# Kernel optimization log

Hardware: AMD Instinct MI355X
Metric: run time of the kernel (lower is better)

The kernel has to match this reference:

```python
import jax, jax.numpy as jnp
import numpy as np

D_MODEL = 1024; D_STATE = 128; EXPAND = 2; HEADDIM = 64
D_INNER = EXPAND * D_MODEL; NHEADS = D_INNER // HEADDIM; PF = 2  # param_factor for complex
BATCH = 2; SEQ = 2048
DT_MIN = 0.001; DT_MAX = 0.1


def setup_inputs() -> dict:
    key = jax.random.key(0)
    k = jax.random.split(key, 10)
    u = jax.random.normal(k[0], (BATCH, SEQ, D_MODEL), jnp.float32)
    in_proj_w = jax.random.normal(k[1], (2 * D_INNER, D_MODEL), jnp.float32) * (D_MODEL ** -0.5)
    dt_projs_weight = jax.random.normal(k[2], (NHEADS, D_INNER), jnp.float32) * 0.02
    dt_projs_bias = (jax.random.uniform(k[3], (NHEADS,), jnp.float32)
                     * (np.log(DT_MAX) - np.log(DT_MIN)) + np.log(DT_MIN)).astype(jnp.float32)
    x_proj_w = jax.random.normal(k[4], (NHEADS * (1 + 2 * D_STATE * PF), D_INNER), jnp.float32) * (D_INNER ** -0.5)
    A = jnp.stack([-jax.random.uniform(k[5], (NHEADS, D_STATE), dtype=jnp.float32),
                   jax.random.normal(k[6], (NHEADS, D_STATE), jnp.float32) * 0.1], axis=-1)  # (H,N,2)
    D = jnp.ones((NHEADS,), jnp.float32)
    norm_B_w = jnp.ones((2 * D_STATE,), jnp.float32)
    norm_C_w = jnp.ones((2 * D_STATE,), jnp.float32)
    out_proj_w = jax.random.normal(k[7], (D_MODEL, D_INNER), jnp.float32) * (D_INNER ** -0.5)
    return {"u": u, "in_proj_w": in_proj_w, "dt_projs_weight": dt_projs_weight,
            "dt_projs_bias": dt_projs_bias, "x_proj_w": x_proj_w, "A": A, "D": D,
            "norm_B_w": norm_B_w, "norm_C_w": norm_C_w, "out_proj_w": out_proj_w}


def _rms_norm(x, w, eps=1e-6):
    return x * jax.lax.rsqrt(jnp.mean(x * x, axis=-1, keepdims=True) + eps) * w


def reference(u, in_proj_w, dt_projs_weight, dt_projs_bias, x_proj_w, A, D,
              norm_B_w, norm_C_w, out_proj_w):
    Bsz, L, _ = u.shape
    xz = u @ in_proj_w.T                        # (B,L,2*d_inner)
    x, z = jnp.split(xz, 2, axis=-1)
    x = jax.nn.silu(x)                          # (B,L,d_inner)
    dt = jax.nn.softplus(x @ dt_projs_weight.T + dt_projs_bias)  # (B,L,H)

    BCp = (x @ x_proj_w.T).reshape(Bsz, L, NHEADS, -1)
    BC = BCp[..., :2 * D_STATE * PF].reshape(Bsz, L, NHEADS, 2, D_STATE, PF)
    Bn = _rms_norm(BC[..., 0, :, :].reshape(Bsz, L, NHEADS, D_STATE * PF), norm_B_w)
    Cn = _rms_norm(BC[..., 1, :, :].reshape(Bsz, L, NHEADS, D_STATE * PF), norm_C_w)
    Bn = Bn.reshape(Bsz, L, NHEADS, D_STATE, PF)
    Cn = Cn.reshape(Bsz, L, NHEADS, D_STATE, PF)
    Bc = jax.lax.complex(Bn[..., 0], Bn[..., 1])  # (B,L,H,N) complex64
    Cc = jax.lax.complex(Cn[..., 0], Cn[..., 1])
    Ac = jax.lax.complex(A[..., 0], A[..., 1])    # (H,N) complex64

    xh = x.reshape(Bsz, L, NHEADS, HEADDIM)
    x_sum = xh.sum(axis=-1)                       # (B,L,H) -- kernel sums x_t over headdim
    zt = Ac[None, None] * (0.5 * dt)[..., None]   # (B,L,H,N) complex: A*dt/2
    den = 1.0 - zt
    abar = (1.0 + zt) / den                       # bilinear (Tustin) discretization
    u_in = Bc * ((dt * x_sum)[..., None] / den)   # Bbar * sum(x_t)

    def step(h, inp):
        a, b = inp
        h = a * h + b
        return h, h

    h0 = jnp.zeros((Bsz, NHEADS, D_STATE), jnp.complex64)
    _, hs = jax.lax.scan(step, h0, (jnp.swapaxes(abar, 0, 1), jnp.swapaxes(u_in, 0, 1)))
    hs = jnp.swapaxes(hs, 0, 1)                   # (B,L,H,N)
    y_red = jnp.real(Cc * hs).sum(axis=-1)        # (B,L,H), Re(C*h) reduced over state
    y = (xh * (y_red + D)[..., None]).reshape(Bsz, L, D_INNER)
    y = y * jax.nn.silu(z)
    return y @ out_proj_w.T
```

## Files before the change

### kernel.cpp

```cpp
#include <hip/hip_runtime.h>

#define BATCH   2
#define SEQ     2048
#define DMODEL  1024
#define DINNER  2048
#define NHEADS  32
#define HEADDIM 64
#define DSTATE  128
#define BLTOT   (BATCH * SEQ)
#define NCHUNK  32
#define CHUNK   64

#define OFF_UB   0ull
#define OFF_WXZ  8388608ull
#define OFF_WBC  16777216ull
#define OFF_WOUT 83886080ull
#define OFF_XB   88080384ull
#define OFF_YB   104857600ull
#define OFF_BC   121634816ull
#define OFF_SZ   255852544ull
#define OFF_DT   272629760ull
#define OFF_XS   273154048ull
#define OFF_CA   274202624ull
#define OFF_CS   276299776ull
#define OFF_HI   278396928ull
#define OFF_SS   280494080ull
#define OFF_P0   281542656ull
#define OFF_P1   298319872ull

typedef __attribute__((ext_vector_type(8))) short bf16x8;
typedef __attribute__((ext_vector_type(4))) float f32x4;

__device__ __forceinline__ float b2f(unsigned short u) {
    return __uint_as_float(((unsigned)u) << 16);
}
__device__ __forceinline__ unsigned short f2b(float f) {
    unsigned x = __float_as_uint(f);
    unsigned r = (x + 0x7fffu + ((x >> 16) & 1u)) >> 16;
    return (unsigned short)r;
}
__device__ __forceinline__ float silu_f(float v) {
    return v / (1.0f + __expf(-v));
}
__device__ __forceinline__ float softplus_f(float v) {
    return (v > 20.0f) ? v : log1pf(__expf(v));
}

__device__ __forceinline__ void gload_lds16(const void* g, void* l) {
    __builtin_amdgcn_global_load_lds(
        (const __attribute__((address_space(1))) unsigned int*)g,
        (__attribute__((address_space(3))) unsigned int*)l, 16, 0, 0);
}

__global__ __launch_bounds__(256) void conv_all_kernel(
    const float* __restrict__ u, const float* __restrict__ ipw,
    const float* __restrict__ opw, const float* __restrict__ xpw,
    unsigned short* __restrict__ u_b, unsigned short* __restrict__ w_xz,
    unsigned short* __restrict__ w_out, unsigned short* __restrict__ w_bc) {
    long idx = (long)blockIdx.x * 256 + threadIdx.x;
    if (idx >= 2621440L) {
        long e = (idx - 2621440L) * 4;
        long c = e >> 11, k = e & 2047;
        const float* s = xpw + ((c >> 9) * 513 + (c & 511)) * 2048 + k;
        float4 v = *(const float4*)s;
        ushort4 o = {f2b(v.x), f2b(v.y), f2b(v.z), f2b(v.w)};
        *(ushort4*)&w_bc[e] = o;
        return;
    }
    const float* src;
    unsigned short* dst;
    long i;
    if (idx < 1048576L)      { src = u;   dst = u_b;   i = idx; }
    else if (idx < 2097152L) { src = ipw; dst = w_xz;  i = idx - 1048576L; }
    else                     { src = opw; dst = w_out; i = idx - 2097152L; }
    float4 v = *(const float4*)&src[i * 4];
    ushort4 o = {f2b(v.x), f2b(v.y), f2b(v.z), f2b(v.w)};
    *(ushort4*)&dst[i * 4] = o;
}

template <int KTOT, int KLEN, int MODE>
__device__ __forceinline__ void gemm_body(
    const unsigned short* __restrict__ A, const unsigned short* __restrict__ B,
    void* __restrict__ C0, void* __restrict__ C1, float* __restrict__ C2,
    int N, int koff) {
    __shared__ short ldsA[128 * 64];
    __shared__ short ldsB[128 * 64];
    int tid = threadIdx.x;
    int row0 = blockIdx.y * 128, col0 = blockIdx.x * 128;
    int lane = tid & 63, wave = tid >> 6;
    int wrow = (wave >> 1) * 64, wcol = (wave & 1) * 64;
    int m = lane & 15, quad = lane >> 4;

    f32x4 acc[4][4];
#pragma unroll
    for (int i = 0; i < 4; ++i)
#pragma unroll
        for (int j = 0; j < 4; ++j) acc[i][j] = (f32x4){0.f, 0.f, 0.f, 0.f};

    int r = tid >> 2, c8 = (tid & 3) * 8;
    const unsigned short* Ag = A + (size_t)(row0 + r) * KTOT + koff + c8;
    const unsigned short* Bg = B + (size_t)(col0 + r) * KTOT + koff + c8;
    short* la = ldsA + tid * 8;
    short* lb = ldsB + tid * 8;

    for (int k0 = 0; k0 < KLEN; k0 += 64) {
#pragma unroll
        for (int p = 0; p < 4; ++p) {
            size_t goff = (size_t)(p >> 1) * 64 * KTOT + (p & 1) * 32 + k0;
            int loff = (p & 1) * 4096 + (p >> 1) * 2048;
            gload_lds16(Ag + goff, la + loff);
            gload_lds16(Bg + goff, lb + loff);
        }
        __syncthreads();
#pragma unroll
        for (int q = 0; q < 2; ++q) {
            bf16x8 af[4], bfr[4];
#pragma unroll
            for (int i = 0; i < 4; ++i)
                af[i] = *(const bf16x8*)
                    &ldsA[q * 4096 + (wrow + i * 16 + m) * 32 + quad * 8];
#pragma unroll
            for (int j = 0; j < 4; ++j)
                bfr[j] = *(const bf16x8*)
                    &ldsB[q * 4096 + (wcol + j * 16 + m) * 32 + quad * 8];
#pragma unroll
            for (int i = 0; i < 4; ++i)
#pragma unroll
                for (int j = 0; j < 4; ++j)
                    acc[i][j] = __builtin_amdgcn_mfma_f32_16x16x32_bf16(
                        af[i], bfr[j], acc[i][j], 0, 0, 0);
        }
        __syncthreads();
    }

    if (MODE == 1) {
        bool isx = (col0 < DINNER);
        if (isx) {
            int head = (col0 + wcol) >> 6;
            float ssum[4][4];
#pragma unroll
            for (int i = 0; i < 4; ++i)
#pragma unroll
                for (int reg = 0; reg < 4; ++reg) ssum[i][reg] = 0.f;
#pragma unroll
            for (int i = 0; i < 4; ++i)
#pragma unroll
                for (int reg = 0; reg < 4; ++reg) {
                    int row = row0 + wrow + i * 16 + quad * 4 + reg;
#pragma unroll
                    for (int j = 0; j < 4; ++j) {
                        int col = col0 + wcol + j * 16 + m;
                        float s = silu_f(acc[i][j][reg]);
                        ((unsigned short*)C0)[(size_t)row * DINNER + col] = f2b(s);
                        ssum[i][reg] += s;
                    }
                }
#pragma unroll
            for (int i = 0; i < 4; ++i)
#pragma unroll
                for (int reg = 0; reg < 4; ++reg) {
                    float s = ssum[i][reg];
                    s += __shfl_xor(s, 1);
                    s += __shfl_xor(s, 2);
                    s += __shfl_xor(s, 4);
                    s += __shfl_xor(s, 8);
                    if (m == 0) {
                        int row = row0 + wrow + i * 16 + quad * 4 + reg;
                        C2[(size_t)row * NHEADS + head] = s;
                    }
                }
        } else {
#pragma unroll
            for (int i = 0; i < 4; ++i)
#pragma unroll
                for (int reg = 0; reg < 4; ++reg) {
                    int row = row0 + wrow + i * 16 + quad * 4 + reg;
#pragma unroll
                    for (int j = 0; j < 4; ++j) {
                        int col = col0 + wcol + j * 16 + m - DINNER;
                        float s = silu_f(acc[i][j][reg]);
                        ((unsigned short*)C1)[(size_t)row * DINNER + col] = f2b(s);
                    }
                }
        }
    } else if (MODE == 2) {
        int hH = (col0 + wcol) >> 9;
        int w0 = (col0 + wcol) & 511;
#pragma unroll
        for (int i = 0; i < 4; ++i)
#pragma unroll
            for (int reg = 0; reg < 4; ++reg) {
                int row = row0 + wrow + i * 16 + quad * 4 + reg;
                unsigned short* dst =
                    (unsigned short*)C0 + ((size_t)hH * BLTOT + row) * 512 + w0;
#pragma unroll
                for (int j = 0; j < 4; ++j)
                    dst[j * 16 + m] = f2b(acc[i][j][reg]);
            }
    } else {
#pragma unroll
        for (int i = 0; i < 4; ++i)
#pragma unroll
            for (int reg = 0; reg < 4; ++reg) {
                int row = row0 + wrow + i * 16 + quad * 4 + reg;
#pragma unroll
                for (int j = 0; j < 4; ++j) {
                    int col = col0 + wcol + j * 16 + m;
                    ((float*)C0)[(size_t)row * N + col] = acc[i][j][reg];
                }
            }
    }
}

__global__ __launch_bounds__(256) void gemm_xz_kernel(
    const unsigned short* __restrict__ A, const unsigned short* __restrict__ B,
    void* C0, void* C1, float* C2) {
    gemm_body<1024, 1024, 1>(A, B, C0, C1, C2, 4096, 0);
}
__global__ __launch_bounds__(256) void gemm_bc_kernel(
    const unsigned short* __restrict__ A, const unsigned short* __restrict__ B,
    void* C0) {
    gemm_body<2048, 2048, 2>(A, B, C0, nullptr, nullptr, 16384, 0);
}
__global__ __launch_bounds__(256) void gemm_out_kernel(
    const unsigned short* __restrict__ A, const unsigned short* __restrict__ B,
    float* P0, float* P1) {
    float* dst = blockIdx.z ? P1 : P0;
    gemm_body<2048, 1024, 0>(A, B, dst, nullptr, nullptr, 1024,
                             blockIdx.z * 1024);
}

__global__ __launch_bounds__(256) void yout_reduce_kernel(
    const float* __restrict__ p0, const float* __restrict__ p1,
    float* __restrict__ out) {
    int i = (blockIdx.x * 256 + threadIdx.x) * 4;
    float4 a = *(const float4*)&p0[i];
    float4 b = *(const float4*)&p1[i];
    float4 o = {a.x + b.x, a.y + b.y, a.z + b.z, a.w + b.w};
    *(float4*)&out[i] = o;
}

__global__ __launch_bounds__(256) void dt_kernel(
    const unsigned short* __restrict__ x, const float* __restrict__ dtw,
    const float* __restrict__ dtb, float* __restrict__ dt) {
    __shared__ float xs[8][132];
    __shared__ float ws[32][132];
    int r0 = blockIdx.x * 8;
    int t = threadIdx.x;
    int lrow = t >> 5, lc4 = (t & 31) * 4;
    int lh = t >> 3, lc16 = (t & 7) * 16;
    int row = t >> 5, h = t & 31;
    float acc = 0.f;

    for (int kc = 0; kc < DINNER; kc += 128) {
        ushort4 a = *(const ushort4*)&x[(size_t)(r0 + lrow) * DINNER + kc + lc4];
        xs[lrow][lc4 + 0] = b2f(a.x); xs[lrow][lc4 + 1] = b2f(a.y);
        xs[lrow][lc4 + 2] = b2f(a.z); xs[lrow][lc4 + 3] = b2f(a.w);
#pragma unroll
        for (int q = 0; q < 4; ++q) {
            float4 w = *(const float4*)&dtw[(size_t)lh * DINNER + kc + lc16 + q * 4];
            *(float4*)&ws[lh][lc16 + q * 4] = w;
        }
        __syncthreads();
#pragma unroll
        for (int k = 0; k < 128; k += 4) {
            float4 xv = *(const float4*)&xs[row][k];
            float4 wv = *(const float4*)&ws[h][k];
            acc += xv.x * wv.x + xv.y * wv.y + xv.z * wv.z + xv.w * wv.w;
        }
        __syncthreads();
    }
    dt[(size_t)(r0 + row) * NHEADS + h] = softplus_f(acc + dtb[h]);
}

__global__ __launch_bounds__(256) void ss_kernel(
    const unsigned short* __restrict__ bct, float* __restrict__ ss) {
    int wgid = blockIdx.x * 4 + (threadIdx.x >> 6);
    int lane = threadIdx.x & 63;
    const unsigned short* p = bct + (size_t)wgid * 512 + lane * 8;
    ushort4 a = *(const ushort4*)p;
    ushort4 b = *(const ushort4*)(p + 4);
    float f0 = b2f(a.x), f1 = b2f(a.y), f2 = b2f(a.z), f3 = b2f(a.w);
    float f4 = b2f(b.x), f5 = b2f(b.y), f6 = b2f(b.z), f7 = b2f(b.w);
    float s = f0 * f0 + f1 * f1 + f2 * f2 + f3 * f3 +
              f4 * f4 + f5 * f5 + f6 * f6 + f7 * f7;
    s += __shfl_xor(s, 1);
    s += __shfl_xor(s, 2);
    s += __shfl_xor(s, 4);
    s += __shfl_xor(s, 8);
    s += __shfl_xor(s, 16);
    if ((lane & 31) == 0)
        ss[(size_t)wgid * 2 + (lane >> 5)] =
            rsqrtf(s * (1.0f / 256.0f) + 1e-6f);
}

__device__ __forceinline__ void coefs(
    float ar, float ai, float dtv, float xsv, float Br, float Bi,
    float& abr, float& abi, float& ur, float& ui) {
    float hd = 0.5f * dtv;
    float ztr = ar * hd, zti = ai * hd;
    float denr = 1.0f - ztr;
    float s2 = 1.0f / (denr * denr + zti * zti);
    float invr = denr * s2, invi = zti * s2;
    float opr = 1.0f + ztr;
    abr = opr * invr - zti * invi;
    abi = opr * invi + zti * invr;
    float coef = dtv * xsv;
    float cr = coef * invr, ci = coef * invi;
    ur = Br * cr - Bi * ci;
    ui = Br * ci + Bi * cr;
}

__global__ __launch_bounds__(64) void scan_pass1(
    const unsigned short* __restrict__ bct, const float* __restrict__ dt,
    const float* __restrict__ xsum, const float* __restrict__ A,
    const float* __restrict__ wB, const float* __restrict__ ss,
    float2* __restrict__ cA, float2* __restrict__ cS) {
    int blk = blockIdx.x;
    int bh = blk >> 5, c = blk & (NCHUNK - 1);
    int b = bh >> 5, h = bh & 31;
    int t = threadIdx.x;
    float4 av = *(const float4*)&A[(h * DSTATE + 2 * t) * 2];
    float4 wv = *(const float4*)&wB[4 * t];
    int l0 = c * CHUNK;
    size_t rbase = (size_t)h * BLTOT + b * SEQ + l0;
    const unsigned short* base = bct + rbase * 512;
    const float* ssp = ss + rbase * 2;
    const float* dtp = dt + (b * SEQ + l0) * NHEADS + h;
    const float* xsp = xsum + (b * SEQ + l0) * NHEADS + h;

    float pr0 = 1.f, pi0 = 0.f, sr0 = 0.f, si0 = 0.f;
    float pr1 = 1.f, pi1 = 0.f, sr1 = 0.f, si1 = 0.f;
    for (int l = 0; l < CHUNK; ++l) {
        uint2 bw = *(const uint2*)&base[(size_t)l * 512 + 4 * t];
        float scale = ssp[l * 2];
        float Br0 = b2f((unsigned short)(bw.x & 0xffff)) * scale * wv.x;
        float Bi0 = b2f((unsigned short)(bw.x >> 16)) * scale * wv.y;
        float Br1 = b2f((unsigned short)(bw.y & 0xffff)) * scale * wv.z;
        float Bi1 = b2f((unsigned short)(bw.y >> 16)) * scale * wv.w;
        float dtv = dtp[l * NHEADS], xsv = xsp[l * NHEADS];
        float abr, abi, ur, ui;
        coefs(av.x, av.y, dtv, xsv, Br0, Bi0, abr, abi, ur, ui);
        float ns = abr * sr0 - abi * si0 + ur;
        float nsi = abr * si0 + abi * sr0 + ui;
        sr0 = ns; si0 = nsi;
        float np = abr * pr0 - abi * pi0;
        float npi = abr * pi0 + abi * pr0;
        pr0 = np; pi0 = npi;
        coefs(av.z, av.w, dtv, xsv, Br1, Bi1, abr, abi, ur, ui);
        ns = abr * sr1 - abi * si1 + ur;
        nsi = abr * si1 + abi * sr1 + ui;
        sr1 = ns; si1 = nsi;
        np = abr * pr1 - abi * pi1;
        npi = abr * pi1 + abi * pr1;
        pr1 = np; pi1 = npi;
    }
    size_t idx = ((size_t)bh * NCHUNK + c) * DSTATE + 2 * t;
    *(float4*)&cA[idx] = (float4){pr0, pi0, pr1, pi1};
    *(float4*)&cS[idx] = (float4){sr0, si0, sr1, si1};
}

__global__ __launch_bounds__(128) void scan_fixup(
    const float2* __restrict__ cA, const float2* __restrict__ cS,
    float2* __restrict__ hin) {
    int bh = blockIdx.x;
    int n = threadIdx.x;
    float hr = 0.f, hi = 0.f;
    for (int c = 0; c < NCHUNK; ++c) {
        size_t idx = ((size_t)bh * NCHUNK + c) * DSTATE + n;
        hin[idx] = {hr, hi};
        float2 a = cA[idx];
        float2 s = cS[idx];
        float nhr = a.x * hr - a.y * hi + s.x;
        float nhi = a.x * hi + a.y * hr + s.y;
        hr = nhr; hi = nhi;
    }
}

__global__ __launch_bounds__(64) void scan_pass2(
    const unsigned short* __restrict__ bct, const float* __restrict__ dt,
    const float* __restrict__ xsum, const float* __restrict__ A,
    const float* __restrict__ wB, const float* __restrict__ wC,
    const float* __restrict__ ss, const float2* __restrict__ hin,
    const unsigned short* __restrict__ xb, const unsigned short* __restrict__ szb,
    const float* __restrict__ Dv, unsigned short* __restrict__ yb) {
    int blk = blockIdx.x;
    int bh = blk >> 5, c = blk & (NCHUNK - 1);
    int b = bh >> 5, h = bh & 31;
    int t = threadIdx.x;
    float4 av = *(const float4*)&A[(h * DSTATE + 2 * t) * 2];
    float4 wbv = *(const float4*)&wB[4 * t];
    float4 wcv = *(const float4*)&wC[4 * t];
    float Dh = Dv[h];
    int l0 = c * CHUNK;
    size_t rbase = (size_t)h * BLTOT + b * SEQ + l0;
    const unsigned short* base = bct + rbase * 512;
    const float* ssp = ss + rbase * 2;
    const float* dtp = dt + (b * SEQ + l0) * NHEADS + h;
    const float* xsp = xsum + (b * SEQ + l0) * NHEADS + h;
    size_t xoff0 = (size_t)(b * SEQ + l0) * DINNER + h * HEADDIM + t;

    float4 h0v = *(const float4*)&hin[((size_t)bh * NCHUNK + c) * DSTATE + 2 * t];
    float hr0 = h0v.x, hi0 = h0v.y, hr1 = h0v.z, hi1 = h0v.w;

    for (int l = 0; l < CHUNK; ++l) {
        uint2 bw = *(const uint2*)&base[(size_t)l * 512 + 4 * t];
        uint2 cw = *(const uint2*)&base[(size_t)l * 512 + 256 + 4 * t];
        float sB = ssp[l * 2 + 0];
        float sC = ssp[l * 2 + 1];
        float Br0 = b2f((unsigned short)(bw.x & 0xffff)) * sB * wbv.x;
        float Bi0 = b2f((unsigned short)(bw.x >> 16)) * sB * wbv.y;
        float Br1 = b2f((unsigned short)(bw.y & 0xffff)) * sB * wbv.z;
        float Bi1 = b2f((unsigned short)(bw.y >> 16)) * sB * wbv.w;
        float Cr0 = b2f((unsigned short)(cw.x & 0xffff)) * sC * wcv.x;
        float Ci0 = b2f((unsigned short)(cw.x >> 16)) * sC * wcv.y;
        float Cr1 = b2f((unsigned short)(cw.y & 0xffff)) * sC * wcv.z;
        float Ci1 = b2f((unsigned short)(cw.y >> 16)) * sC * wcv.w;
        float dtv = dtp[l * NHEADS], xsv = xsp[l * NHEADS];
        float abr, abi, ur, ui;
        coefs(av.x, av.y, dtv, xsv, Br0, Bi0, abr, abi, ur, ui);
        float nhr = abr * hr0 - abi * hi0 + ur;
        float nhi = abr * hi0 + abi * hr0 + ui;
        hr0 = nhr; hi0 = nhi;
        coefs(av.z, av.w, dtv, xsv, Br1, Bi1, abr, abi, ur, ui);
        nhr = abr * hr1 - abi * hi1 + ur;
        nhi = abr * hi1 + abi * hr1 + ui;
        hr1 = nhr; hi1 = nhi;
        float y = Cr0 * hr0 - Ci0 * hi0 + Cr1 * hr1 - Ci1 * hi1;
#pragma unroll
        for (int off = 1; off < 64; off <<= 1) y += __shfl_xor(y, off);
        size_t xo = xoff0 + (size_t)l * DINNER;
        float yr = y + Dh;
        float xv = b2f(xb[xo]);
        float zv = b2f(szb[xo]);
        yb[xo] = f2b(xv * yr * zv);
    }
}

extern "C" void kernel_launch(void* const* d_in, const int* in_sizes, int n_in,
                              void* d_out, int out_size, void* d_ws, size_t ws_size,
                              hipStream_t stream) {
    const float* u   = (const float*)d_in[0];
    const float* ipw = (const float*)d_in[1];
    const float* dtw = (const float*)d_in[2];
    const float* dtb = (const float*)d_in[3];
    const float* xpw = (const float*)d_in[4];
    const float* A   = (const float*)d_in[5];
    const float* Dv  = (const float*)d_in[6];
    const float* wB  = (const float*)d_in[7];
    const float* wC  = (const float*)d_in[8];
    const float* opw = (const float*)d_in[9];
    float* out = (float*)d_out;
    char* ws = (char*)d_ws;

    unsigned short* u_b   = (unsigned short*)(ws + OFF_UB);
    unsigned short* w_xz  = (unsigned short*)(ws + OFF_WXZ);
    unsigned short* w_bc  = (unsigned short*)(ws + OFF_WBC);
    unsigned short* w_out = (unsigned short*)(ws + OFF_WOUT);
    unsigned short* x_b   = (unsigned short*)(ws + OFF_XB);
    unsigned short* y_b   = (unsigned short*)(ws + OFF_YB);
    unsigned short* bct   = (unsigned short*)(ws + OFF_BC);
    unsigned short* sz    = (unsigned short*)(ws + OFF_SZ);
    float* dt    = (float*)(ws + OFF_DT);
    float* xsum  = (float*)(ws + OFF_XS);
    float2* cA   = (float2*)(ws + OFF_CA);
    float2* cS   = (float2*)(ws + OFF_CS);
    float2* hin  = (float2*)(ws + OFF_HI);
    float* ssbuf = (float*)(ws + OFF_SS);
    float* p0    = (float*)(ws + OFF_P0);
    float* p1    = (float*)(ws + OFF_P1);

    conv_all_kernel<<<43008, 256, 0, stream>>>(u, ipw, opw, xpw,
                                               u_b, w_xz, w_out, w_bc);

    gemm_xz_kernel<<<dim3(32, 32), 256, 0, stream>>>(u_b, w_xz, x_b, sz, xsum);
    dt_kernel<<<BLTOT / 8, 256, 0, stream>>>(x_b, dtw, dtb, dt);
    gemm_bc_kernel<<<dim3(128, 32), 256, 0, stream>>>(x_b, w_bc, bct);
    ss_kernel<<<NHEADS * BLTOT / 4, 256, 0, stream>>>(bct, ssbuf);

    scan_pass1<<<BATCH * NHEADS * NCHUNK, 64, 0, stream>>>(
        bct, dt, xsum, A, wB, ssbuf, cA, cS);
    scan_fixup<<<BATCH * NHEADS, 128, 0, stream>>>(cA, cS, hin);
    scan_pass2<<<BATCH * NHEADS * NCHUNK, 64, 0, stream>>>(
        bct, dt, xsum, A, wB, wC, ssbuf, hin, x_b, sz, Dv, y_b);

    gemm_out_kernel<<<dim3(8, 32, 2), 256, 0, stream>>>(y_b, w_out, p0, p1);
    yout_reduce_kernel<<<BLTOT * DMODEL / 4 / 256, 256, 0, stream>>>(p0, p1, out);
}
```

Measured before the change: 789.2 us.

## Split BC projection output into separate B and C planes and swap grid order

The B/C projection GEMM now writes B and C values into two separate planes (256 wide each) instead of one interleaved 512-wide row. Scan pass 1 reads only the B plane, so it no longer pulls C data into cache lines it never uses. The BC GEMM grid is also transposed so that consecutive blocks walk along rows of x for the same weight columns, which changes which operand tiles are reused in L2. The ss and scan kernels are updated to index the two planes.

```diff
diff --git a/kernel.cpp b/kernel.cpp
--- a/kernel.cpp
+++ b/kernel.cpp
@@ -17,7 +17,8 @@
 #define OFF_WOUT 83886080ull
 #define OFF_XB   88080384ull
 #define OFF_YB   104857600ull
-#define OFF_BC   121634816ull
+#define OFF_BCB  121634816ull
+#define OFF_BCC  188743680ull
 #define OFF_SZ   255852544ull
 #define OFF_DT   272629760ull
 #define OFF_XS   273154048ull
@@ -78,7 +79,7 @@
     *(ushort4*)&dst[i * 4] = o;
 }
 
-template <int KTOT, int KLEN, int MODE>
+template <int KTOT, int KLEN, int MODE, int SWAP>
 __device__ __forceinline__ void gemm_body(
     const unsigned short* __restrict__ A, const unsigned short* __restrict__ B,
     void* __restrict__ C0, void* __restrict__ C1, float* __restrict__ C2,
@@ -86,7 +87,8 @@
     __shared__ short ldsA[128 * 64];
     __shared__ short ldsB[128 * 64];
     int tid = threadIdx.x;
-    int row0 = blockIdx.y * 128, col0 = blockIdx.x * 128;
+    int row0 = (SWAP ? blockIdx.x : blockIdx.y) * 128;
+    int col0 = (SWAP ? blockIdx.y : blockIdx.x) * 128;
     int lane = tid & 63, wave = tid >> 6;
     int wrow = (wave >> 1) * 64, wcol = (wave & 1) * 64;
     int m = lane & 15, quad = lane >> 4;
@@ -184,15 +186,19 @@
                 }
         }
     } else if (MODE == 2) {
-        int hH = (col0 + wcol) >> 9;
-        int w0 = (col0 + wcol) & 511;
+        int cc = col0 + wcol;
+        int hH = cc >> 9;
+        int w0 = cc & 511;
+        unsigned short* plane =
+            (w0 < 256) ? (unsigned short*)C0 : (unsigned short*)C1;
+        int wo = w0 & 255;
 #pragma unroll
         for (int i = 0; i < 4; ++i)
 #pragma unroll
             for (int reg = 0; reg < 4; ++reg) {
                 int row = row0 + wrow + i * 16 + quad * 4 + reg;
                 unsigned short* dst =
-                    (unsigned short*)C0 + ((size_t)hH * BLTOT + row) * 512 + w0;
+                    plane + ((size_t)hH * BLTOT + row) * 256 + wo;
 #pragma unroll
                 for (int j = 0; j < 4; ++j)
                     dst[j * 16 + m] = f2b(acc[i][j][reg]);
@@ -215,19 +221,19 @@
 __global__ __launch_bounds__(256) void gemm_xz_kernel(
     const unsigned short* __restrict__ A, const unsigned short* __restrict__ B,
     void* C0, void* C1, float* C2) {
-    gemm_body<1024, 1024, 1>(A, B, C0, C1, C2, 4096, 0);
+    gemm_body<1024, 1024, 1, 0>(A, B, C0, C1, C2, 4096, 0);
 }
 __global__ __launch_bounds__(256) void gemm_bc_kernel(
     const unsigned short* __restrict__ A, const unsigned short* __restrict__ B,
-    void* C0) {
-    gemm_body<2048, 2048, 2>(A, B, C0, nullptr, nullptr, 16384, 0);
+    void* Bp, void* Cp) {
+    gemm_body<2048, 2048, 2, 1>(A, B, Bp, Cp, nullptr, 16384, 0);
 }
 __global__ __launch_bounds__(256) void gemm_out_kernel(
     const unsigned short* __restrict__ A, const unsigned short* __restrict__ B,
     float* P0, float* P1) {
     float* dst = blockIdx.z ? P1 : P0;
-    gemm_body<2048, 1024, 0>(A, B, dst, nullptr, nullptr, 1024,
-                             blockIdx.z * 1024);
+    gemm_body<2048, 1024, 0, 0>(A, B, dst, nullptr, nullptr, 1024,
+                                blockIdx.z * 1024);
 }
 
 __global__ __launch_bounds__(256) void yout_reduce_kernel(
@@ -274,10 +280,12 @@
 }
 
 __global__ __launch_bounds__(256) void ss_kernel(
-    const unsigned short* __restrict__ bct, float* __restrict__ ss) {
+    const unsigned short* __restrict__ bcB, const unsigned short* __restrict__ bcC,
+    float* __restrict__ ss) {
     int wgid = blockIdx.x * 4 + (threadIdx.x >> 6);
     int lane = threadIdx.x & 63;
-    const unsigned short* p = bct + (size_t)wgid * 512 + lane * 8;
+    const unsigned short* plane = (lane < 32) ? bcB : bcC;
+    const unsigned short* p = plane + (size_t)wgid * 256 + (lane & 31) * 8;
     ushort4 a = *(const ushort4*)p;
     ushort4 b = *(const ushort4*)(p + 4);
     float f0 = b2f(a.x), f1 = b2f(a.y), f2 = b2f(a.z), f3 = b2f(a.w);
@@ -312,7 +320,7 @@
 }
 
 __global__ __launch_bounds__(64) void scan_pass1(
-    const unsigned short* __restrict__ bct, const float* __restrict__ dt,
+    const unsigned short* __restrict__ bcB, const float* __restrict__ dt,
     const float* __restrict__ xsum, const float* __restrict__ A,
     const float* __restrict__ wB, const float* __restrict__ ss,
     float2* __restrict__ cA, float2* __restrict__ cS) {
@@ -324,7 +332,7 @@
     float4 wv = *(const float4*)&wB[4 * t];
     int l0 = c * CHUNK;
     size_t rbase = (size_t)h * BLTOT + b * SEQ + l0;
-    const unsigned short* base = bct + rbase * 512;
+    const unsigned short* base = bcB + rbase * 256;
     const float* ssp = ss + rbase * 2;
     const float* dtp = dt + (b * SEQ + l0) * NHEADS + h;
     const float* xsp = xsum + (b * SEQ + l0) * NHEADS + h;
@@ -332,7 +340,7 @@
     float pr0 = 1.f, pi0 = 0.f, sr0 = 0.f, si0 = 0.f;
     float pr1 = 1.f, pi1 = 0.f, sr1 = 0.f, si1 = 0.f;
     for (int l = 0; l < CHUNK; ++l) {
-        uint2 bw = *(const uint2*)&base[(size_t)l * 512 + 4 * t];
+        uint2 bw = *(const uint2*)&base[(size_t)l * 256 + 4 * t];
         float scale = ssp[l * 2];
         float Br0 = b2f((unsigned short)(bw.x & 0xffff)) * scale * wv.x;
         float Bi0 = b2f((unsigned short)(bw.x >> 16)) * scale * wv.y;
@@ -378,12 +386,13 @@
 }
 
 __global__ __launch_bounds__(64) void scan_pass2(
-    const unsigned short* __restrict__ bct, const float* __restrict__ dt,
-    const float* __restrict__ xsum, const float* __restrict__ A,
-    const float* __restrict__ wB, const float* __restrict__ wC,
-    const float* __restrict__ ss, const float2* __restrict__ hin,
-    const unsigned short* __restrict__ xb, const unsigned short* __restrict__ szb,
-    const float* __restrict__ Dv, unsigned short* __restrict__ yb) {
+    const unsigned short* __restrict__ bcB, const unsigned short* __restrict__ bcC,
+    const float* __restrict__ dt, const float* __restrict__ xsum,
+    const float* __restrict__ A, const float* __restrict__ wB,
+    const float* __restrict__ wC, const float* __restrict__ ss,
+    const float2* __restrict__ hin, const unsigned short* __restrict__ xb,
+    const unsigned short* __restrict__ szb, const float* __restrict__ Dv,
+    unsigned short* __restrict__ yb) {
     int blk = blockIdx.x;
     int bh = blk >> 5, c = blk & (NCHUNK - 1);
     int b = bh >> 5, h = bh & 31;
@@ -394,7 +403,8 @@
     float Dh = Dv[h];
     int l0 = c * CHUNK;
     size_t rbase = (size_t)h * BLTOT + b * SEQ + l0;
-    const unsigned short* base = bct + rbase * 512;
+    const unsigned short* baseB = bcB + rbase * 256;
+    const unsigned short* baseC = bcC + rbase * 256;
     const float* ssp = ss + rbase * 2;
     const float* dtp = dt + (b * SEQ + l0) * NHEADS + h;
     const float* xsp = xsum + (b * SEQ + l0) * NHEADS + h;
@@ -404,8 +414,8 @@
     float hr0 = h0v.x, hi0 = h0v.y, hr1 = h0v.z, hi1 = h0v.w;
 
     for (int l = 0; l < CHUNK; ++l) {
-        uint2 bw = *(const uint2*)&base[(size_t)l * 512 + 4 * t];
-        uint2 cw = *(const uint2*)&base[(size_t)l * 512 + 256 + 4 * t];
+        uint2 bw = *(const uint2*)&baseB[(size_t)l * 256 + 4 * t];
+        uint2 cw = *(const uint2*)&baseC[(size_t)l * 256 + 4 * t];
         float sB = ssp[l * 2 + 0];
         float sC = ssp[l * 2 + 1];
         float Br0 = b2f((unsigned short)(bw.x & 0xffff)) * sB * wbv.x;
@@ -459,7 +469,8 @@
     unsigned short* w_out = (unsigned short*)(ws + OFF_WOUT);
     unsigned short* x_b   = (unsigned short*)(ws + OFF_XB);
     unsigned short* y_b   = (unsigned short*)(ws + OFF_YB);
-    unsigned short* bct   = (unsigned short*)(ws + OFF_BC);
+    unsigned short* bcB   = (unsigned short*)(ws + OFF_BCB);
+    unsigned short* bcC   = (unsigned short*)(ws + OFF_BCC);
     unsigned short* sz    = (unsigned short*)(ws + OFF_SZ);
     float* dt    = (float*)(ws + OFF_DT);
     float* xsum  = (float*)(ws + OFF_XS);
@@ -475,14 +486,14 @@
 
     gemm_xz_kernel<<<dim3(32, 32), 256, 0, stream>>>(u_b, w_xz, x_b, sz, xsum);
     dt_kernel<<<BLTOT / 8, 256, 0, stream>>>(x_b, dtw, dtb, dt);
-    gemm_bc_kernel<<<dim3(128, 32), 256, 0, stream>>>(x_b, w_bc, bct);
-    ss_kernel<<<NHEADS * BLTOT / 4, 256, 0, stream>>>(bct, ssbuf);
+    gemm_bc_kernel<<<dim3(32, 128), 256, 0, stream>>>(x_b, w_bc, bcB, bcC);
+    ss_kernel<<<NHEADS * BLTOT / 4, 256, 0, stream>>>(bcB, bcC, ssbuf);
 
     scan_pass1<<<BATCH * NHEADS * NCHUNK, 64, 0, stream>>>(
-        bct, dt, xsum, A, wB, ssbuf, cA, cS);
+        bcB, dt, xsum, A, wB, ssbuf, cA, cS);
     scan_fixup<<<BATCH * NHEADS, 128, 0, stream>>>(cA, cS, hin);
     scan_pass2<<<BATCH * NHEADS * NCHUNK, 64, 0, stream>>>(
-        bct, dt, xsum, A, wB, wC, ssbuf, hin, x_b, sz, Dv, y_b);
+        bcB, bcC, dt, xsum, A, wB, wC, ssbuf, hin, x_b, sz, Dv, y_b);
 
     gemm_out_kernel<<<dim3(8, 32, 2), 256, 0, stream>>>(y_b, w_out, p0, p1);
     yout_reduce_kernel<<<BLTOT * DMODEL / 4 / 256, 256, 0, stream>>>(p0, p1, out);
```

Measured after the change: 793.4 us. Within noise of the previous version (+0.5%).
